# Performance work log

Hardware: AMD Instinct MI355X
Metric: run time of the kernel (lower is better)

## Reference

```python
import jax, jax.numpy as jnp
import numpy as np

B, S, D_IN, HID = 64, 512, 1024, 4096  # HID = 4 * state_size
HS = HID // 4


def setup_inputs() -> dict:
    key = jax.random.key(0)
    k1, k2, k3 = jax.random.split(key, 3)
    x = jax.random.normal(k1, (B, S, D_IN), dtype=jnp.float32)
    wx = jax.random.uniform(k2, (HID, D_IN), minval=-0.1, maxval=0.1, dtype=jnp.float32)
    wh = jax.random.uniform(k3, (HID, HS), minval=-0.1, maxval=0.1, dtype=jnp.float32)
    bx = jnp.zeros((HID,), dtype=jnp.float32)
    bh = jnp.zeros((HID,), dtype=jnp.float32)
    return {"x": x, "wx": wx, "wh": wh, "bx": bx, "bh": bh}


def _lstm(x, wx, wh, bx, bh):
    batch = x.shape[0]
    hs = wh.shape[1]
    # Precompute the input contribution for all timesteps in one big GEMM.
    # xg: [S, B, HID]
    xg = jnp.einsum('bsd,gd->sbg', x, wx) + bx + bh

    def step(carry, xg_t):
        h, c = carry
        gates = xg_t + h @ wh.T  # [B, HID]
        i, f, g, o = jnp.split(gates, 4, axis=1)
        i = jax.nn.sigmoid(i)
        f = jax.nn.sigmoid(f)
        g = jnp.tanh(g)
        o = jax.nn.sigmoid(o)
        c = f * c + i * g
        h = o * jnp.tanh(c)
        return (h, c), h

    h0 = jnp.zeros((batch, hs), dtype=x.dtype)
    c0 = jnp.zeros((batch, hs), dtype=x.dtype)
    (h, c), hs_seq = jax.lax.scan(step, (h0, c0), xg)
    out = jnp.transpose(hs_seq, (1, 0, 2))  # [B, S, HS]
    return out, (h, c)


def reference(x, wx, wh, bx, bh):
    return _lstm(x, wx, wh, bx, bh)
```

## Files before the change

kernel.cpp:

```cpp
#include <hip/hip_runtime.h>
#include <hip/hip_bf16.h>
#include <stdint.h>


typedef __attribute__((ext_vector_type(8))) short short8;
typedef __attribute__((ext_vector_type(4))) float floatx4;

#define S_LEN 512
#define BATCH 64
#define DIN   1024
#define HID   4096
#define HS    1024

#define XG2_OFF   0ull
#define XBF_OFF   268435456ull
#define WXBF_OFF  335544320ull
#define WHBF_OFF  343932928ull
#define HBUF_OFF  352321536ull
#define FLAG_OFF  352583680ull

__device__ __forceinline__ unsigned short f2bf(float f) {
  unsigned int u = __float_as_uint(f);
  u += 0x7fffu + ((u >> 16) & 1u);
  return (unsigned short)(u >> 16);
}
__device__ __forceinline__ float bf2f(unsigned short s) {
  return __uint_as_float(((unsigned int)s) << 16);
}

__device__ __forceinline__ void async_ld16(const void* g, const void* l) {
  __builtin_amdgcn_global_load_lds(
      (const __attribute__((address_space(1))) unsigned int*)g,
      (__attribute__((address_space(3))) unsigned int*)l,
      16, 0, 0);
}

__device__ __forceinline__ short8 load16_llc(const void* p) {
  floatx4 r;
  asm volatile("global_load_dwordx4 %0, %1, off sc0 sc1"
               : "=v"(r) : "v"(p) : "memory");
  return __builtin_bit_cast(short8, r);
}
__device__ __forceinline__ void store2_llc(void* p, unsigned int v) {
  asm volatile("global_store_short %0, %1, off sc0 sc1"
               :: "v"(p), "v"(v) : "memory");
}
__device__ __forceinline__ void wait_vm0() {
  asm volatile("s_waitcnt vmcnt(0)" ::: "memory");
}

__device__ __forceinline__ float sigmoidf_(float x) {
  return 1.0f / (1.0f + __expf(-x));
}
__device__ __forceinline__ float tanhf_(float x) {
  return 2.0f / (1.0f + __expf(-2.0f * x)) - 1.0f;
}

__global__ void cvt_kernel(const float* __restrict__ src,
                           unsigned short* __restrict__ dst, int n4) {
  int i = blockIdx.x * blockDim.x + threadIdx.x;
  if (i < n4) {
    float4 v = ((const float4*)src)[i];
    ushort4 o;
    o.x = f2bf(v.x); o.y = f2bf(v.y); o.z = f2bf(v.z); o.w = f2bf(v.w);
    ((ushort4*)dst)[i] = o;
  }
}

__global__ void zero_kernel(unsigned int* __restrict__ p, int n) {
  int i = blockIdx.x * blockDim.x + threadIdx.x;
  if (i < n) p[i] = 0u;
}

__global__ __launch_bounds__(256) void pregemm_kernel(
    const unsigned short* __restrict__ A,
    const unsigned short* __restrict__ Bw,
    const float* __restrict__ bx, const float* __restrict__ bh,
    unsigned short* __restrict__ xg2) {
  __shared__ unsigned short As[128 * 32];
  __shared__ unsigned short Bs[128 * 32];
  const int tid = threadIdx.x;
  const int lane = tid & 63, wv = tid >> 6;
  const int l15 = lane & 15, lq = lane >> 4;
  const int m0 = blockIdx.y * 128, n0 = blockIdx.x * 128;
  const int wm = (wv >> 1) * 64, wn = (wv & 1) * 64;

  floatx4 acc[4][4];
#pragma unroll
  for (int i = 0; i < 4; i++)
#pragma unroll
    for (int j = 0; j < 4; j++) acc[i][j] = (floatx4){0.f, 0.f, 0.f, 0.f};

  for (int k0 = 0; k0 < DIN; k0 += 32) {
#pragma unroll
    for (int q = 0; q < 2; q++) {
      const int e = (q * 256 + tid) * 8;
      const int r = e >> 5, c = e & 31;
      async_ld16(A + (size_t)(m0 + r) * DIN + k0 + c, (unsigned short*)As + e);
      async_ld16(Bw + (size_t)(n0 + r) * DIN + k0 + c, (unsigned short*)Bs + e);
    }
    __syncthreads();
    short8 af[4], bfv[4];
#pragma unroll
    for (int i = 0; i < 4; i++)
      af[i] = *(const short8*)&As[(wm + i * 16 + l15) * 32 + lq * 8];
#pragma unroll
    for (int j = 0; j < 4; j++)
      bfv[j] = *(const short8*)&Bs[(wn + j * 16 + l15) * 32 + lq * 8];
#pragma unroll
    for (int i = 0; i < 4; i++)
#pragma unroll
      for (int j = 0; j < 4; j++)
        acc[i][j] = __builtin_amdgcn_mfma_f32_16x16x32_bf16(af[i], bfv[j],
                                                            acc[i][j], 0, 0, 0);
    __syncthreads();
  }

#pragma unroll
  for (int j = 0; j < 4; j++) {
    const int col = n0 + wn + j * 16 + l15;
    const float bias = bx[col] + bh[col];
    const int gate = col >> 10;
    const int c1 = col & 1023;
    const int wslice = c1 >> 4, cc = c1 & 15;
    const int n_idx = gate * 16 + cc;
#pragma unroll
    for (int i = 0; i < 4; i++) {
#pragma unroll
      for (int r = 0; r < 4; r++) {
        const int m = m0 + wm + i * 16 + lq * 4 + r;
        const int b = m >> 9, t = m & 511;
        const size_t idx =
            ((size_t)(t * 256 + ((b >> 4) * 64 + wslice)) * 16 + (b & 15)) * 64 +
            n_idx;
        xg2[idx] = f2bf(acc[i][j][r] + bias);
      }
    }
  }
}

__global__ __launch_bounds__(256, 1) void lstm_kernel(
    const unsigned short* __restrict__ whbf,
    const unsigned short* __restrict__ xg2,
    unsigned short* __restrict__ hbuf,
    int* __restrict__ flags,
    float* __restrict__ out,
    float* __restrict__ outh, float* __restrict__ outc) {
  __shared__ float gpart[4 * 16 * 68];

  const int tid = threadIdx.x;
  const int lane = tid & 63, kq = tid >> 6;
  const int l15 = lane & 15, lq = lane >> 4;
  const int wg = blockIdx.x;
  const int group = wg >> 6, wslice = wg & 63;
  const int j0 = wslice * 16;

  short8 bfrag[4][8];
#pragma unroll
  for (int j = 0; j < 4; j++) {
    const size_t grow = (size_t)(j * 1024 + j0 + l15) * HS;
#pragma unroll
    for (int kc = 0; kc < 8; kc++)
      bfrag[j][kc] = *(const short8*)&whbf[grow + kq * 256 + kc * 32 + lq * 8];
  }

  const int eb = tid >> 4;
  const int ec = tid & 15;
  const int gb = group * 16 + eb;
  float c_state = 0.0f;

  const int arow = (group * 16 + l15) * HS + kq * 256 + lq * 8;
  int* fp = flags + (size_t)(group * 64 + kq * 16 + l15) * 16;

  for (int t = 0; t < S_LEN; t++) {
    if (t > 0) {
      while (true) {
        int v = t;
        if (lq == 0)
          v = __hip_atomic_load(fp, __ATOMIC_RELAXED, __HIP_MEMORY_SCOPE_AGENT);
        if (__all(v >= t)) break;
        __builtin_amdgcn_s_sleep(2);
      }
    }

    const unsigned short* xr = xg2 + ((size_t)(t * 256 + wg) * 16 + eb) * 64 + ec;
    const unsigned short xv0 = xr[0], xv1 = xr[16], xv2 = xr[32], xv3 = xr[48];

    const unsigned short* hp = hbuf + (size_t)(t & 1) * (BATCH * HS) + arow;
    short8 a[8];
#pragma unroll
    for (int kc = 0; kc < 8; kc++) a[kc] = load16_llc(&hp[kc * 32]);
    asm volatile("s_waitcnt vmcnt(0)"
                 : "+v"(a[0]), "+v"(a[1]), "+v"(a[2]), "+v"(a[3]),
                   "+v"(a[4]), "+v"(a[5]), "+v"(a[6]), "+v"(a[7])
                 :: "memory");

    floatx4 acc0 = (floatx4){0.f, 0.f, 0.f, 0.f};
    floatx4 acc1 = acc0, acc2 = acc0, acc3 = acc0;
#pragma unroll
    for (int kc = 0; kc < 8; kc++) {
      acc0 = __builtin_amdgcn_mfma_f32_16x16x32_bf16(a[kc], bfrag[0][kc], acc0, 0, 0, 0);
      acc1 = __builtin_amdgcn_mfma_f32_16x16x32_bf16(a[kc], bfrag[1][kc], acc1, 0, 0, 0);
      acc2 = __builtin_amdgcn_mfma_f32_16x16x32_bf16(a[kc], bfrag[2][kc], acc2, 0, 0, 0);
      acc3 = __builtin_amdgcn_mfma_f32_16x16x32_bf16(a[kc], bfrag[3][kc], acc3, 0, 0, 0);
    }
#pragma unroll
    for (int r = 0; r < 4; r++) {
      const int row = (kq * 16 + lq * 4 + r) * 68;
      gpart[row + 0 * 16 + l15] = acc0[r];
      gpart[row + 1 * 16 + l15] = acc1[r];
      gpart[row + 2 * 16 + l15] = acc2[r];
      gpart[row + 3 * 16 + l15] = acc3[r];
    }
    __syncthreads();

    float g0 = bf2f(xv0), g1 = bf2f(xv1), g2 = bf2f(xv2), g3 = bf2f(xv3);
#pragma unroll
    for (int q = 0; q < 4; q++) {
      const float* gp = &gpart[(q * 16 + eb) * 68 + ec];
      g0 += gp[0]; g1 += gp[16]; g2 += gp[32]; g3 += gp[48];
    }
    const float i_ = sigmoidf_(g0);
    const float f_ = sigmoidf_(g1);
    const float gg = tanhf_(g2);
    const float o_ = sigmoidf_(g3);
    c_state = f_ * c_state + i_ * gg;
    const float h = o_ * tanhf_(c_state);

    store2_llc(&hbuf[(size_t)((t + 1) & 1) * (BATCH * HS) + gb * HS + j0 + ec],
               (unsigned int)f2bf(h));
    __builtin_nontemporal_store(h, &out[((size_t)gb * S_LEN + t) * HS + j0 + ec]);

    if (t == S_LEN - 1) {
      outh[gb * HS + j0 + ec] = h;
      outc[gb * HS + j0 + ec] = c_state;
      break;
    }

    wait_vm0();
    __syncthreads();
    if (tid == 0)
      __hip_atomic_store(&flags[wg * 16], t + 1, __ATOMIC_RELAXED,
                         __HIP_MEMORY_SCOPE_AGENT);
  }
}

extern "C" void kernel_launch(void* const* d_in, const int* in_sizes, int n_in,
                              void* d_out, int out_size, void* d_ws,
                              size_t ws_size, hipStream_t stream) {
  const float* x  = (const float*)d_in[0];
  const float* wx = (const float*)d_in[1];
  const float* wh = (const float*)d_in[2];
  const float* bx = (const float*)d_in[3];
  const float* bh = (const float*)d_in[4];
  char* ws = (char*)d_ws;
  unsigned short* xg2  = (unsigned short*)(ws + XG2_OFF);
  unsigned short* xbf  = (unsigned short*)(ws + XBF_OFF);
  unsigned short* wxbf = (unsigned short*)(ws + WXBF_OFF);
  unsigned short* whbf = (unsigned short*)(ws + WHBF_OFF);
  unsigned short* hbuf = (unsigned short*)(ws + HBUF_OFF);
  int* flags = (int*)(ws + FLAG_OFF);

  float* out  = (float*)d_out;
  float* outh = out + (size_t)BATCH * S_LEN * HS;
  float* outc = outh + BATCH * HS;

  cvt_kernel<<<(33554432 / 4) / 256, 256, 0, stream>>>(x, xbf, 33554432 / 4);
  cvt_kernel<<<(4194304 / 4) / 256, 256, 0, stream>>>(wx, wxbf, 4194304 / 4);
  cvt_kernel<<<(4194304 / 4) / 256, 256, 0, stream>>>(wh, whbf, 4194304 / 4);
  zero_kernel<<<(69632 + 255) / 256, 256, 0, stream>>>(
      (unsigned int*)(ws + HBUF_OFF), 69632);

  dim3 pg(HID / 128, (BATCH * S_LEN) / 128);
  pregemm_kernel<<<pg, 256, 0, stream>>>(xbf, wxbf, bx, bh, xg2);

  lstm_kernel<<<256, 256, 0, stream>>>(whbf, xg2, hbuf, flags, out, outh, outc);
}
```

Baseline: 2.360 ms.

## Replace per-block flags with step-tagged hidden-state words for inter-block sync

Each hidden value is now stored as a 32-bit word carrying the bf16 value in the low half and the timestep tag in the high half. Consumers spin directly on the hidden-state loads until every tag matches the current step, which removes the separate flag store, the vmcnt wait before it, and the extra flag-poll round trip. The next step's xg values are also prefetched one iteration ahead. In exchange the hidden buffer doubles in size, each poll rereads the full operand set, and the buffer reuses the xbf workspace region after the pre-GEMM finishes.

```diff
diff --git a/kernel.cpp b/kernel.cpp
--- a/kernel.cpp
+++ b/kernel.cpp
@@ -5,6 +5,7 @@
 
 typedef __attribute__((ext_vector_type(8))) short short8;
 typedef __attribute__((ext_vector_type(4))) float floatx4;
+typedef __attribute__((ext_vector_type(4))) unsigned int uintx4;
 
 #define S_LEN 512
 #define BATCH 64
@@ -16,8 +17,7 @@
 #define XBF_OFF   268435456ull
 #define WXBF_OFF  335544320ull
 #define WHBF_OFF  343932928ull
-#define HBUF_OFF  352321536ull
-#define FLAG_OFF  352583680ull
+#define HBUF32_OFF XBF_OFF
 
 __device__ __forceinline__ unsigned short f2bf(float f) {
   unsigned int u = __float_as_uint(f);
@@ -26,6 +26,9 @@
 }
 __device__ __forceinline__ float bf2f(unsigned short s) {
   return __uint_as_float(((unsigned int)s) << 16);
+}
+__device__ __forceinline__ unsigned int umin_(unsigned int a, unsigned int b) {
+  return a < b ? a : b;
 }
 
 __device__ __forceinline__ void async_ld16(const void* g, const void* l) {
@@ -35,18 +38,9 @@
       16, 0, 0);
 }
 
-__device__ __forceinline__ short8 load16_llc(const void* p) {
-  floatx4 r;
-  asm volatile("global_load_dwordx4 %0, %1, off sc0 sc1"
-               : "=v"(r) : "v"(p) : "memory");
-  return __builtin_bit_cast(short8, r);
-}
-__device__ __forceinline__ void store2_llc(void* p, unsigned int v) {
-  asm volatile("global_store_short %0, %1, off sc0 sc1"
+__device__ __forceinline__ void st4_llc(void* p, unsigned int v) {
+  asm volatile("global_store_dword %0, %1, off sc0 sc1"
                :: "v"(p), "v"(v) : "memory");
-}
-__device__ __forceinline__ void wait_vm0() {
-  asm volatile("s_waitcnt vmcnt(0)" ::: "memory");
 }
 
 __device__ __forceinline__ float sigmoidf_(float x) {
@@ -142,8 +136,7 @@
 __global__ __launch_bounds__(256, 1) void lstm_kernel(
     const unsigned short* __restrict__ whbf,
     const unsigned short* __restrict__ xg2,
-    unsigned short* __restrict__ hbuf,
-    int* __restrict__ flags,
+    unsigned int* __restrict__ hbuf32,
     float* __restrict__ out,
     float* __restrict__ outh, float* __restrict__ outc) {
   __shared__ float gpart[4 * 16 * 68];
@@ -169,31 +162,61 @@
   const int gb = group * 16 + eb;
   float c_state = 0.0f;
 
-  const int arow = (group * 16 + l15) * HS + kq * 256 + lq * 8;
-  int* fp = flags + (size_t)(group * 64 + kq * 16 + l15) * 16;
+  const size_t arow = (size_t)(group * 16 + l15) * HS + kq * 256 + lq * 8;
+
+  const unsigned short* xr0 = xg2 + ((size_t)(0 * 256 + wg) * 16 + eb) * 64 + ec;
+  unsigned short xv0 = xr0[0], xv1 = xr0[16], xv2 = xr0[32], xv3 = xr0[48];
 
   for (int t = 0; t < S_LEN; t++) {
+    uintx4 qa[16];
     if (t > 0) {
+      const unsigned int* hp = hbuf32 + (size_t)(t & 1) * (BATCH * HS) + arow;
       while (true) {
-        int v = t;
-        if (lq == 0)
-          v = __hip_atomic_load(fp, __ATOMIC_RELAXED, __HIP_MEMORY_SCOPE_AGENT);
-        if (__all(v >= t)) break;
-        __builtin_amdgcn_s_sleep(2);
+#pragma unroll
+        for (int kc = 0; kc < 8; kc++) {
+          asm volatile("global_load_dwordx4 %0, %1, off sc0 sc1"
+                       : "=v"(qa[2 * kc]) : "v"(hp + kc * 32) : "memory");
+          asm volatile("global_load_dwordx4 %0, %1, off sc0 sc1"
+                       : "=v"(qa[2 * kc + 1]) : "v"(hp + kc * 32 + 4) : "memory");
+        }
+        asm volatile("s_waitcnt vmcnt(0)"
+                     : "+v"(qa[0]), "+v"(qa[1]), "+v"(qa[2]), "+v"(qa[3]),
+                       "+v"(qa[4]), "+v"(qa[5]), "+v"(qa[6]), "+v"(qa[7])
+                     :: "memory");
+        asm volatile(""
+                     : "+v"(qa[8]), "+v"(qa[9]), "+v"(qa[10]), "+v"(qa[11]),
+                       "+v"(qa[12]), "+v"(qa[13]), "+v"(qa[14]), "+v"(qa[15])
+                     :: "memory");
+        unsigned int mn = 0xffffffffu;
+#pragma unroll
+        for (int i = 0; i < 16; i++) {
+          unsigned int m1 = umin_(umin_(qa[i].x, qa[i].y),
+                                  umin_(qa[i].z, qa[i].w));
+          mn = umin_(mn, m1);
+        }
+        if (__all((int)(mn >> 16) == t)) break;
+        __builtin_amdgcn_s_sleep(1);
       }
-    }
-
-    const unsigned short* xr = xg2 + ((size_t)(t * 256 + wg) * 16 + eb) * 64 + ec;
-    const unsigned short xv0 = xr[0], xv1 = xr[16], xv2 = xr[32], xv3 = xr[48];
-
-    const unsigned short* hp = hbuf + (size_t)(t & 1) * (BATCH * HS) + arow;
+    } else {
+#pragma unroll
+      for (int i = 0; i < 16; i++) qa[i] = (uintx4){0u, 0u, 0u, 0u};
+    }
+
+    const unsigned short* xb =
+        xg2 + ((size_t)((t + 1) * 256 + wg) * 16 + eb) * 64 + ec;
+    unsigned short nx0 = xb[0], nx1 = xb[16], nx2 = xb[32], nx3 = xb[48];
+
     short8 a[8];
 #pragma unroll
-    for (int kc = 0; kc < 8; kc++) a[kc] = load16_llc(&hp[kc * 32]);
-    asm volatile("s_waitcnt vmcnt(0)"
-                 : "+v"(a[0]), "+v"(a[1]), "+v"(a[2]), "+v"(a[3]),
-                   "+v"(a[4]), "+v"(a[5]), "+v"(a[6]), "+v"(a[7])
-                 :: "memory");
+    for (int kc = 0; kc < 8; kc++) {
+      const uintx4 lo = qa[2 * kc], hi = qa[2 * kc + 1];
+      uintx4 w;
+      w.x = __builtin_amdgcn_perm(lo.y, lo.x, 0x05040100u);
+      w.y = __builtin_amdgcn_perm(lo.w, lo.z, 0x05040100u);
+      w.z = __builtin_amdgcn_perm(hi.y, hi.x, 0x05040100u);
+      w.w = __builtin_amdgcn_perm(hi.w, hi.z, 0x05040100u);
+      a[kc] = __builtin_bit_cast(short8, w);
+    }
 
     floatx4 acc0 = (floatx4){0.f, 0.f, 0.f, 0.f};
     floatx4 acc1 = acc0, acc2 = acc0, acc3 = acc0;
@@ -227,21 +250,22 @@
     c_state = f_ * c_state + i_ * gg;
     const float h = o_ * tanhf_(c_state);
 
-    store2_llc(&hbuf[(size_t)((t + 1) & 1) * (BATCH * HS) + gb * HS + j0 + ec],
-               (unsigned int)f2bf(h));
-    __builtin_nontemporal_store(h, &out[((size_t)gb * S_LEN + t) * HS + j0 + ec]);
+    st4_llc(&hbuf32[(size_t)((t + 1) & 1) * (BATCH * HS) + (size_t)gb * HS +
+                    j0 + ec],
+            (((unsigned int)(t + 1)) << 16) | (unsigned int)f2bf(h));
 
     if (t == S_LEN - 1) {
+      out[((size_t)gb * S_LEN + t) * HS + j0 + ec] = h;
       outh[gb * HS + j0 + ec] = h;
       outc[gb * HS + j0 + ec] = c_state;
       break;
     }
 
-    wait_vm0();
+    __builtin_nontemporal_store(h, &out[((size_t)gb * S_LEN + t) * HS + j0 + ec]);
+
     __syncthreads();
-    if (tid == 0)
-      __hip_atomic_store(&flags[wg * 16], t + 1, __ATOMIC_RELAXED,
-                         __HIP_MEMORY_SCOPE_AGENT);
+
+    xv0 = nx0; xv1 = nx1; xv2 = nx2; xv3 = nx3;
   }
 }
 
@@ -258,8 +282,7 @@
   unsigned short* xbf  = (unsigned short*)(ws + XBF_OFF);
   unsigned short* wxbf = (unsigned short*)(ws + WXBF_OFF);
   unsigned short* whbf = (unsigned short*)(ws + WHBF_OFF);
-  unsigned short* hbuf = (unsigned short*)(ws + HBUF_OFF);
-  int* flags = (int*)(ws + FLAG_OFF);
+  unsigned int*   hbuf32 = (unsigned int*)(ws + HBUF32_OFF);
 
   float* out  = (float*)d_out;
   float* outh = out + (size_t)BATCH * S_LEN * HS;
@@ -268,11 +291,11 @@
   cvt_kernel<<<(33554432 / 4) / 256, 256, 0, stream>>>(x, xbf, 33554432 / 4);
   cvt_kernel<<<(4194304 / 4) / 256, 256, 0, stream>>>(wx, wxbf, 4194304 / 4);
   cvt_kernel<<<(4194304 / 4) / 256, 256, 0, stream>>>(wh, whbf, 4194304 / 4);
-  zero_kernel<<<(69632 + 255) / 256, 256, 0, stream>>>(
-      (unsigned int*)(ws + HBUF_OFF), 69632);
 
   dim3 pg(HID / 128, (BATCH * S_LEN) / 128);
   pregemm_kernel<<<pg, 256, 0, stream>>>(xbf, wxbf, bx, bh, xg2);
 
-  lstm_kernel<<<256, 256, 0, stream>>>(whbf, xg2, hbuf, flags, out, outh, outc);
-}
+  zero_kernel<<<(131072 + 255) / 256, 256, 0, stream>>>(hbuf32, 131072);
+
+  lstm_kernel<<<256, 256, 0, stream>>>(whbf, xg2, hbuf32, out, outh, outc);
+}
```

Result: slower. 2.663 ms (+12.9%).

## Use per-wave step flags and prefetch next-step gate inputs in persistent LSTM

Applied to the files above, without the earlier changes.

Each wave now publishes its own completion flag through a cache-bypassing store right after its h stores drain, instead of a block barrier followed by one thread's atomic flag write. Consumers poll four per-wave flags per producer with LLC loads. The next timestep's precomputed input gates and the output store are issued before the trailing barrier so their latency overlaps the synchronisation. The flag region is moved into the reused xbf workspace and zeroed after the pre-GEMM, and polling sleep is shortened. This trades more flag traffic and polling load for a shorter critical path per recurrent step.

```diff
diff --git a/kernel.cpp b/kernel.cpp
--- a/kernel.cpp
+++ b/kernel.cpp
@@ -17,7 +17,7 @@
 #define WXBF_OFF  335544320ull
 #define WHBF_OFF  343932928ull
 #define HBUF_OFF  352321536ull
-#define FLAG_OFF  352583680ull
+#define FLAG_OFF  XBF_OFF
 
 __device__ __forceinline__ unsigned short f2bf(float f) {
   unsigned int u = __float_as_uint(f);
@@ -45,8 +45,16 @@
   asm volatile("global_store_short %0, %1, off sc0 sc1"
                :: "v"(p), "v"(v) : "memory");
 }
-__device__ __forceinline__ void wait_vm0() {
-  asm volatile("s_waitcnt vmcnt(0)" ::: "memory");
+__device__ __forceinline__ void st4_llc(void* p, unsigned int v) {
+  asm volatile("global_store_dword %0, %1, off sc0 sc1"
+               :: "v"(p), "v"(v) : "memory");
+}
+__device__ __forceinline__ int ld_flag_llc(const int* p) {
+  int v;
+  asm volatile("global_load_dword %0, %1, off sc0 sc1\n\t"
+               "s_waitcnt vmcnt(0)"
+               : "=v"(v) : "v"(p) : "memory");
+  return v;
 }
 
 __device__ __forceinline__ float sigmoidf_(float x) {
@@ -169,22 +177,21 @@
   const int gb = group * 16 + eb;
   float c_state = 0.0f;
 
-  const int arow = (group * 16 + l15) * HS + kq * 256 + lq * 8;
-  int* fp = flags + (size_t)(group * 64 + kq * 16 + l15) * 16;
+  const size_t arow = (size_t)(group * 16 + l15) * HS + kq * 256 + lq * 8;
+  const int* fp = flags +
+      ((size_t)((group * 64 + kq * 16 + (lane >> 2)) * 4 + (lane & 3))) * 16;
+
+  const unsigned short* xr0 = xg2 + ((size_t)(0 * 256 + wg) * 16 + eb) * 64 + ec;
+  unsigned short xv0 = xr0[0], xv1 = xr0[16], xv2 = xr0[32], xv3 = xr0[48];
 
   for (int t = 0; t < S_LEN; t++) {
     if (t > 0) {
       while (true) {
-        int v = t;
-        if (lq == 0)
-          v = __hip_atomic_load(fp, __ATOMIC_RELAXED, __HIP_MEMORY_SCOPE_AGENT);
+        int v = ld_flag_llc(fp);
         if (__all(v >= t)) break;
-        __builtin_amdgcn_s_sleep(2);
+        __builtin_amdgcn_s_sleep(1);
       }
     }
-
-    const unsigned short* xr = xg2 + ((size_t)(t * 256 + wg) * 16 + eb) * 64 + ec;
-    const unsigned short xv0 = xr[0], xv1 = xr[16], xv2 = xr[32], xv3 = xr[48];
 
     const unsigned short* hp = hbuf + (size_t)(t & 1) * (BATCH * HS) + arow;
     short8 a[8];
@@ -227,21 +234,30 @@
     c_state = f_ * c_state + i_ * gg;
     const float h = o_ * tanhf_(c_state);
 
-    store2_llc(&hbuf[(size_t)((t + 1) & 1) * (BATCH * HS) + gb * HS + j0 + ec],
+    store2_llc(&hbuf[(size_t)((t + 1) & 1) * (BATCH * HS) + (size_t)gb * HS +
+                     j0 + ec],
                (unsigned int)f2bf(h));
-    __builtin_nontemporal_store(h, &out[((size_t)gb * S_LEN + t) * HS + j0 + ec]);
 
     if (t == S_LEN - 1) {
+      out[((size_t)gb * S_LEN + t) * HS + j0 + ec] = h;
       outh[gb * HS + j0 + ec] = h;
       outc[gb * HS + j0 + ec] = c_state;
       break;
     }
 
-    wait_vm0();
-    __syncthreads();
-    if (tid == 0)
-      __hip_atomic_store(&flags[wg * 16], t + 1, __ATOMIC_RELAXED,
-                         __HIP_MEMORY_SCOPE_AGENT);
+    asm volatile("s_waitcnt vmcnt(0)" ::: "memory");
+    if (lane == 0)
+      st4_llc(&flags[(wg * 4 + kq) * 16], (unsigned int)(t + 1));
+
+    const unsigned short* xb =
+        xg2 + ((size_t)((t + 1) * 256 + wg) * 16 + eb) * 64 + ec;
+    unsigned short nx0 = xb[0], nx1 = xb[16], nx2 = xb[32], nx3 = xb[48];
+
+    __builtin_nontemporal_store(h, &out[((size_t)gb * S_LEN + t) * HS + j0 + ec]);
+
+    __syncthreads();
+
+    xv0 = nx0; xv1 = nx1; xv2 = nx2; xv3 = nx3;
   }
 }
 
@@ -268,11 +284,12 @@
   cvt_kernel<<<(33554432 / 4) / 256, 256, 0, stream>>>(x, xbf, 33554432 / 4);
   cvt_kernel<<<(4194304 / 4) / 256, 256, 0, stream>>>(wx, wxbf, 4194304 / 4);
   cvt_kernel<<<(4194304 / 4) / 256, 256, 0, stream>>>(wh, whbf, 4194304 / 4);
-  zero_kernel<<<(69632 + 255) / 256, 256, 0, stream>>>(
-      (unsigned int*)(ws + HBUF_OFF), 69632);
+  zero_kernel<<<256, 256, 0, stream>>>((unsigned int*)(ws + HBUF_OFF), 65536);
 
   dim3 pg(HID / 128, (BATCH * S_LEN) / 128);
   pregemm_kernel<<<pg, 256, 0, stream>>>(xbf, wxbf, bx, bh, xg2);
 
+  zero_kernel<<<64, 256, 0, stream>>>((unsigned int*)flags, 16384);
+
   lstm_kernel<<<256, 256, 0, stream>>>(whbf, xg2, hbuf, flags, out, outh, outc);
 }
```

After: 2.130 ms. 9.7% less time.
